# Optimization experiments

Measured on AMD Instinct MI355X. Metric: run time of the kernel, lower is better.

## Reference

```python
import jax, jax.numpy as jnp
import numpy as np

B, LC, LE, D, M = 128, 256, 1024, 256, 512
NEG = -1e9


def setup_inputs() -> dict:
    key = jax.random.key(0)
    ks = jax.random.split(key, 10)
    s = 0.02
    return {
        "criteria": jax.random.normal(ks[0], (B, LC, D), jnp.float32),
        "ehr": jax.random.normal(ks[1], (B, LE, D), jnp.float32),
        "criteria_mask": jax.random.randint(ks[2], (B, LC), 0, 2, jnp.int32),
        "ehr_mask": jax.random.randint(ks[3], (B, LE), 0, 2, jnp.int32),
        # params stored (in, out); torch Linear is x @ W.T + b
        "Wa": jax.random.normal(ks[4], (D, D), jnp.float32) * s,
        "ba": jnp.zeros((D,), jnp.float32),
        "Wr": jax.random.normal(ks[5], (2 * D, D), jnp.float32) * s,
        "br": jnp.zeros((D,), jnp.float32),
        "Wm": jax.random.normal(ks[6], (4 * D, M), jnp.float32) * s,
        "bm": jnp.zeros((M,), jnp.float32),
        "Wo": jax.random.normal(ks[7], (M, 3), jnp.float32) * s,
        "bo": jnp.zeros((3,), jnp.float32),
    }


def reference(criteria, ehr, Wa, ba, Wr, br, Wm, bm, Wo, bo,
              criteria_mask, ehr_mask):
    relu = jax.nn.relu
    c = relu(criteria @ Wa + ba)              # (B, Lc, D)
    e = relu(ehr @ Wa + ba)                   # (B, Le, D)
    align = jnp.einsum("bld,bed->ble", c, e)  # (B, Lc, Le)

    cm = criteria_mask.astype(align.dtype)
    em = ehr_mask.astype(align.dtype)
    # beta: softmax over Lc (dim=1), masked by criteria_mask along Lc
    beta = jax.nn.softmax(align + (1.0 - cm)[:, :, None] * NEG, axis=1)
    # alpha: softmax over Le (dim=1 of transposed), masked by ehr_mask along Le
    alpha = jax.nn.softmax(align + (1.0 - em)[:, None, :] * NEG, axis=2)

    # (alpha.unsqueeze(-1) * ehr.unsqueeze(1)).sum(2) == alpha @ ehr
    att_c = jnp.einsum("ble,bed->bld", alpha, ehr)        # (B, Lc, D)
    r1 = relu(jnp.concatenate([att_c, criteria], axis=-1) @ Wr + br).sum(axis=1)  # (B, D)

    # (beta.unsqueeze(-1) * criteria.unsqueeze(2)).sum(1) == beta.T @ criteria
    att_e = jnp.einsum("ble,bld->bed", beta, criteria)    # (B, Le, D)
    r2 = relu(jnp.concatenate([att_e, ehr], axis=-1) @ Wr + br).sum(axis=1)       # (B, D)

    m = jnp.concatenate([r1, r2, r1 * r2, r1 - r2], axis=-1)  # (B, 4D)
    return relu(m @ Wm + bm) @ Wo + bo                        # (B, 3)
```

## Files before the change

### kernel.cpp

```cpp
#include <hip/hip_runtime.h>
#include <hip/hip_bf16.h>

#define BB 128
#define LC 256
#define LE 1024
#define DD 256
#define MM 512

typedef short bf16x8 __attribute__((ext_vector_type(8)));
typedef unsigned short u16x8 __attribute__((ext_vector_type(8)));
typedef unsigned short u16x4 __attribute__((ext_vector_type(4)));
typedef float f32x4 __attribute__((ext_vector_type(4)));

__device__ __forceinline__ float bfu2f(unsigned short u) {
  return __uint_as_float(((unsigned int)u) << 16);
}
__device__ __forceinline__ unsigned short f2bfu(float f) {
  unsigned int x = __float_as_uint(f);
  return (unsigned short)((x + 0x7fffu + ((x >> 16) & 1u)) >> 16);
}

#define LDST 40
__device__ __forceinline__ int ldsoff(int r, int q) {
  return r * LDST + ((q ^ ((r >> 2) & 3)) << 3);
}

__device__ __forceinline__ void mma_step(const unsigned short* As, const unsigned short* Bs,
                                         f32x4 (&acc)[4][4], int wm, int wn, int lane) {
  const int lm = lane & 15, quad = lane >> 4;
  bf16x8 a[4], b[4];
#pragma unroll
  for (int i = 0; i < 4; ++i) {
    int r = wm * 64 + i * 16 + lm;
    a[i] = *(const bf16x8*)&As[ldsoff(r, quad)];
    int n = wn * 64 + i * 16 + lm;
    b[i] = *(const bf16x8*)&Bs[ldsoff(n, quad)];
  }
#pragma unroll
  for (int i = 0; i < 4; ++i)
#pragma unroll
    for (int j = 0; j < 4; ++j)
      acc[i][j] = __builtin_amdgcn_mfma_f32_16x16x32_bf16(a[i], b[j], acc[i][j], 0, 0, 0);
}

template <int MT, int NT>
__device__ __forceinline__ void mma_tiles(const unsigned short* As, const unsigned short* Bs,
                                          f32x4 (&acc)[MT][NT], int m0, int n0, int lane) {
  const int lm = lane & 15, quad = lane >> 4;
  bf16x8 a[MT], b[NT];
#pragma unroll
  for (int i = 0; i < MT; ++i)
    a[i] = *(const bf16x8*)&As[ldsoff(m0 + i * 16 + lm, quad)];
#pragma unroll
  for (int j = 0; j < NT; ++j)
    b[j] = *(const bf16x8*)&Bs[ldsoff(n0 + j * 16 + lm, quad)];
#pragma unroll
  for (int i = 0; i < MT; ++i)
#pragma unroll
    for (int j = 0; j < NT; ++j)
      acc[i][j] = __builtin_amdgcn_mfma_f32_16x16x32_bf16(a[i], b[j], acc[i][j], 0, 0, 0);
}

__device__ __forceinline__ void stage_bf16(unsigned short* S, const unsigned short* g,
                                           long ld, int tid) {
#pragma unroll
  for (int i = 0; i < 2; ++i) {
    int c = tid + i * 256;
    int r = c >> 2, q = c & 3;
    u16x8 v = *(const u16x8*)(g + (long)r * ld + q * 8);
    *(u16x8*)&S[ldsoff(r, q)] = v;
  }
}

__device__ __forceinline__ void stage_f32(unsigned short* S, const float* g, long ld, int tid) {
#pragma unroll
  for (int i = 0; i < 2; ++i) {
    int c = tid + i * 256;
    int r = c >> 2, q = c & 3;
    const float4* p = (const float4*)(g + (long)r * ld + q * 8);
    float4 v0 = p[0], v1 = p[1];
    u16x8 o;
    o[0] = f2bfu(v0.x); o[1] = f2bfu(v0.y); o[2] = f2bfu(v0.z); o[3] = f2bfu(v0.w);
    o[4] = f2bfu(v1.x); o[5] = f2bfu(v1.y); o[6] = f2bfu(v1.z); o[7] = f2bfu(v1.w);
    *(u16x8*)&S[ldsoff(r, q)] = o;
  }
}

__device__ __forceinline__ void stage512(unsigned short* S, const unsigned short* g,
                                         long ld, int tid) {
  int r = tid >> 2, q = tid & 3;
  *(u16x8*)&S[ldsoff(r, q)] = *(const u16x8*)(g + (long)r * ld + q * 8);
}

__device__ __forceinline__ void stage512x2(unsigned short* S, const unsigned short* g,
                                           long ld, int tid) {
#pragma unroll
  for (int it = 0; it < 2; ++it) {
    int c = tid + it * 512;
    int r = c >> 2, q = c & 3;
    *(u16x8*)&S[ldsoff(r, q)] = *(const u16x8*)(g + (long)r * ld + q * 8);
  }
}

__global__ void zero_kernel(float* __restrict__ p, int n) {
  int i = blockIdx.x * 256 + threadIdx.x;
  if (i < n) p[i] = 0.f;
}

__global__ void wconv_kernel(const float* __restrict__ Wa, const float* __restrict__ Wr,
                             unsigned short* __restrict__ WaT, unsigned short* __restrict__ WrT) {
  int i = blockIdx.x * 256 + threadIdx.x;
  if (i < 65536) WaT[i] = f2bfu(Wa[(i & 255) * 256 + (i >> 8)]);
  if (i < 131072) WrT[i] = f2bfu(Wr[(long)(i & 511) * 256 + (i >> 9)]);
}

__global__ void transT_kernel(const float* __restrict__ src, const int* __restrict__ mask,
                              unsigned short* __restrict__ dstT, unsigned short* __restrict__ dstN,
                              int R, int C) {
  __shared__ unsigned short T[64][72];
  const int tid = threadIdx.x, b = blockIdx.z;
  const int r0 = blockIdx.y * 64, c0 = blockIdx.x * 64;
  const float* s = src + (long)b * R * C;
  const int* mk = mask + (long)b * R;
  unsigned short* dT = dstT + (long)b * R * C;
  unsigned short* dN = dstN + (long)b * R * C;
#pragma unroll
  for (int i = 0; i < 4; ++i) {
    int r = (tid >> 4) + i * 16, c4 = tid & 15;
    float4 v = *(const float4*)(s + (long)(r0 + r) * C + c0 + c4 * 4);
    u16x4 nat;
    nat[0] = f2bfu(v.x); nat[1] = f2bfu(v.y); nat[2] = f2bfu(v.z); nat[3] = f2bfu(v.w);
    *(u16x4*)(dN + (long)(r0 + r) * C + c0 + c4 * 4) = nat;
    float g = mk[r0 + r] ? 1.f : 0.f;
    T[c4 * 4 + 0][r] = f2bfu(v.x * g);
    T[c4 * 4 + 1][r] = f2bfu(v.y * g);
    T[c4 * 4 + 2][r] = f2bfu(v.z * g);
    T[c4 * 4 + 3][r] = f2bfu(v.w * g);
  }
  __syncthreads();
#pragma unroll
  for (int j = 0; j < 2; ++j) {
    int idx = tid * 2 + j;
    int row = idx >> 3, ch = idx & 7;
    *(u16x8*)(dT + (long)(c0 + row) * R + r0 + ch * 8) = *(const u16x8*)&T[row][ch * 8];
  }
}

__global__ __launch_bounds__(256, 2) void proj_mfma(const float* __restrict__ A,
                                                    const unsigned short* __restrict__ WaT,
                                                    const float* __restrict__ ba,
                                                    unsigned short* __restrict__ out) {
  __shared__ unsigned short As[128 * LDST], Bs[128 * LDST];
  const int tid = threadIdx.x, lane = tid & 63, w = tid >> 6, wm = w >> 1, wn = w & 1;
  const long m0 = (long)blockIdx.y * 128;
  const int n0 = blockIdx.x * 128;
  f32x4 acc[4][4] = {};
  for (int k0 = 0; k0 < DD; k0 += 32) {
    stage_f32(As, A + m0 * DD + k0, DD, tid);
    stage_bf16(Bs, WaT + (long)n0 * DD + k0, DD, tid);
    __syncthreads();
    mma_step(As, Bs, acc, wm, wn, lane);
    __syncthreads();
  }
  const int lm = lane & 15, quad = lane >> 4;
#pragma unroll
  for (int i = 0; i < 4; ++i)
#pragma unroll
    for (int j = 0; j < 4; ++j) {
      int col = n0 + wn * 64 + j * 16 + lm;
      float bias = ba[col];
#pragma unroll
      for (int r = 0; r < 4; ++r) {
        long row = m0 + wm * 64 + i * 16 + quad * 4 + r;
        float v = acc[i][j][r] + bias;
        out[row * DD + col] = f2bfu(v > 0.f ? v : 0.f);
      }
    }
}

__global__ __launch_bounds__(512, 2) void attn_c_fused(
    const unsigned short* __restrict__ cB, const unsigned short* __restrict__ eB,
    const unsigned short* __restrict__ ehrTm, const int* __restrict__ em,
    unsigned short* __restrict__ attc) {
  __shared__ unsigned short AB[256 * LDST];
  __shared__ unsigned short S4[4][128 * LDST];
  __shared__ float asum_s[128];
  const int tid = threadIdx.x, lane = tid & 63, w = tid >> 6;
  const int lm = lane & 15, quad = lane >> 4;
  const int wmS = w >> 2, wnS = w & 3;
  const int wm = w >> 2, wn = w & 3;
  const int fid = blockIdx.x;
  const int lid = (fid & 7) * 32 + (fid >> 3);
  const int b = lid >> 1, m0 = (lid & 1) * 128;
  unsigned short* As = AB;
  unsigned short* Bs = AB + 128 * LDST;
  const unsigned short* Ag = cB + ((long)b * LC + m0) * DD;
  if (tid < 128) asum_s[tid] = 0.f;
  f32x4 acc[4][4] = {};
  float ap0 = 0.f, ap1 = 0.f;
  __syncthreads();
  for (int ch = 0; ch < 8; ++ch) {
    const unsigned short* Eg = eB + ((long)b * LE + ch * 128) * DD;
    f32x4 accS[4][2] = {};
    for (int k0 = 0; k0 < DD; k0 += 32) {
      stage512(As, Eg + k0, DD, tid);
      stage512(Bs, Ag + k0, DD, tid);
      __syncthreads();
      mma_tiles<4, 2>(As, Bs, accS, wmS * 64, wnS * 32, lane);
      __syncthreads();
    }
#pragma unroll
    for (int i = 0; i < 4; ++i) {
      const int Le0 = wmS * 64 + i * 16 + quad * 4;
      const int4 m4 = *(const int4*)(em + (long)b * LE + ch * 128 + Le0);
      const float em0 = m4.x ? 1.f : 0.f, em1 = m4.y ? 1.f : 0.f;
      const float em2 = m4.z ? 1.f : 0.f, em3 = m4.w ? 1.f : 0.f;
      const int kk = Le0 >> 5, wi = Le0 & 31;
      const int qq = wi >> 3, sub = wi & 7;
#pragma unroll
      for (int j = 0; j < 2; ++j) {
        const int row = wnS * 32 + j * 16 + lm;
        float e0 = __expf(accS[i][j][0]);
        float e1 = __expf(accS[i][j][1]);
        float e2 = __expf(accS[i][j][2]);
        float e3 = __expf(accS[i][j][3]);
        float s = em0 * e0 + em1 * e1 + em2 * e2 + em3 * e3;
        if (j == 0) ap0 += s; else ap1 += s;
        u16x4 pk;
        pk[0] = f2bfu(e0); pk[1] = f2bfu(e1); pk[2] = f2bfu(e2); pk[3] = f2bfu(e3);
        *(u16x4*)&S4[kk][ldsoff(row, qq) + sub] = pk;
      }
    }
    __syncthreads();
    for (int kk = 0; kk < 4; ++kk) {
      stage512x2(AB, ehrTm + (long)b * DD * LE + ch * 128 + kk * 32, LE, tid);
      __syncthreads();
      mma_tiles<4, 4>(&S4[kk][0], AB, acc, wm * 64, wn * 64, lane);
      __syncthreads();
    }
  }
  {
    float s = ap0;
    s += __shfl_xor(s, 16); s += __shfl_xor(s, 32);
    if (quad == 0) atomicAdd(&asum_s[wnS * 32 + 0 * 16 + lm], s);
    float t = ap1;
    t += __shfl_xor(t, 16); t += __shfl_xor(t, 32);
    if (quad == 0) atomicAdd(&asum_s[wnS * 32 + 1 * 16 + lm], t);
  }
  __syncthreads();
  float rs[4][4];
#pragma unroll
  for (int i = 0; i < 4; ++i)
#pragma unroll
    for (int r = 0; r < 4; ++r)
      rs[i][r] = 1.f / asum_s[wm * 64 + i * 16 + quad * 4 + r];
#pragma unroll
  for (int i = 0; i < 4; ++i)
#pragma unroll
    for (int j = 0; j < 4; ++j) {
      int col = wn * 64 + j * 16 + lm;
#pragma unroll
      for (int r = 0; r < 4; ++r) {
        int row = wm * 64 + i * 16 + quad * 4 + r;
        attc[((long)b * LC + m0 + row) * DD + col] = f2bfu(acc[i][j][r] * rs[i][r]);
      }
    }
}

__global__ __launch_bounds__(512, 2) void attn_e_fused(
    const unsigned short* __restrict__ cB, const unsigned short* __restrict__ eB,
    const unsigned short* __restrict__ critTm, const int* __restrict__ cm,
    unsigned short* __restrict__ atte) {
  __shared__ unsigned short AB[256 * LDST];
  __shared__ unsigned short S4[4][128 * LDST];
  __shared__ float bsum_s[128];
  const int tid = threadIdx.x, lane = tid & 63, w = tid >> 6;
  const int lm = lane & 15, quad = lane >> 4;
  const int wmS = w >> 2, wnS = w & 3;
  const int wm = w >> 2, wn = w & 3;
  const int fid = blockIdx.x;
  const int lid = (fid & 7) * 128 + (fid >> 3);
  const int b = lid >> 3, n0 = (lid & 7) * 128;
  unsigned short* As = AB;
  unsigned short* Bs = AB + 128 * LDST;
  const unsigned short* Eg = eB + ((long)b * LE + n0) * DD;
  if (tid < 128) bsum_s[tid] = 0.f;
  f32x4 acc[4][4] = {};
  float bp0 = 0.f, bp1 = 0.f;
  __syncthreads();
  for (int ch = 0; ch < 2; ++ch) {
    const unsigned short* Cg = cB + ((long)b * LC + ch * 128) * DD;
    f32x4 accS[4][2] = {};
    for (int k0 = 0; k0 < DD; k0 += 32) {
      stage512(As, Cg + k0, DD, tid);
      stage512(Bs, Eg + k0, DD, tid);
      __syncthreads();
      mma_tiles<4, 2>(As, Bs, accS, wmS * 64, wnS * 32, lane);
      __syncthreads();
    }
#pragma unroll
    for (int i = 0; i < 4; ++i) {
      const int Lc0 = wmS * 64 + i * 16 + quad * 4;
      const int4 m4 = *(const int4*)(cm + (long)b * LC + ch * 128 + Lc0);
      const float cm0 = m4.x ? 1.f : 0.f, cm1 = m4.y ? 1.f : 0.f;
      const float cm2 = m4.z ? 1.f : 0.f, cm3 = m4.w ? 1.f : 0.f;
      const int kk = Lc0 >> 5, wi = Lc0 & 31;
      const int qq = wi >> 3, sub = wi & 7;
#pragma unroll
      for (int j = 0; j < 2; ++j) {
        const int row = wnS * 32 + j * 16 + lm;
        float e0 = __expf(accS[i][j][0]);
        float e1 = __expf(accS[i][j][1]);
        float e2 = __expf(accS[i][j][2]);
        float e3 = __expf(accS[i][j][3]);
        float s = cm0 * e0 + cm1 * e1 + cm2 * e2 + cm3 * e3;
        if (j == 0) bp0 += s; else bp1 += s;
        u16x4 pk;
        pk[0] = f2bfu(e0); pk[1] = f2bfu(e1); pk[2] = f2bfu(e2); pk[3] = f2bfu(e3);
        *(u16x4*)&S4[kk][ldsoff(row, qq) + sub] = pk;
      }
    }
    __syncthreads();
    for (int kk = 0; kk < 4; ++kk) {
      stage512x2(AB, critTm + (long)b * DD * LC + ch * 128 + kk * 32, LC, tid);
      __syncthreads();
      mma_tiles<4, 4>(&S4[kk][0], AB, acc, wm * 64, wn * 64, lane);
      __syncthreads();
    }
  }
  {
    float s = bp0;
    s += __shfl_xor(s, 16); s += __shfl_xor(s, 32);
    if (quad == 0) atomicAdd(&bsum_s[wnS * 32 + 0 * 16 + lm], s);
    float t = bp1;
    t += __shfl_xor(t, 16); t += __shfl_xor(t, 32);
    if (quad == 0) atomicAdd(&bsum_s[wnS * 32 + 1 * 16 + lm], t);
  }
  __syncthreads();
  float rs[4][4];
#pragma unroll
  for (int i = 0; i < 4; ++i)
#pragma unroll
    for (int r = 0; r < 4; ++r)
      rs[i][r] = 1.f / bsum_s[wm * 64 + i * 16 + quad * 4 + r];
#pragma unroll
  for (int i = 0; i < 4; ++i)
#pragma unroll
    for (int j = 0; j < 4; ++j) {
      int col = wn * 64 + j * 16 + lm;
#pragma unroll
      for (int r = 0; r < 4; ++r) {
        int row = wm * 64 + i * 16 + quad * 4 + r;
        atte[((long)b * LE + n0 + row) * DD + col] = f2bfu(acc[i][j][r] * rs[i][r]);
      }
    }
}

__global__ __launch_bounds__(256, 2) void rsum_mfma(const unsigned short* __restrict__ att,
                                                    const unsigned short* __restrict__ origB,
                                                    const unsigned short* __restrict__ WrT,
                                                    const float* __restrict__ br,
                                                    float* __restrict__ rout, int Lseq) {
  __shared__ unsigned short As[128 * LDST], Bs[128 * LDST];
  __shared__ float red[2][128];
  const int tid = threadIdx.x, lane = tid & 63, w = tid >> 6, wm = w >> 1, wn = w & 1;
  const long m0 = (long)blockIdx.y * 128;
  const int n0 = blockIdx.x * 128;
  const int b = (int)(m0 / Lseq);
  f32x4 acc[4][4] = {};
  for (int k0 = 0; k0 < 2 * DD; k0 += 32) {
    if (k0 < DD)
      stage_bf16(As, att + m0 * DD + k0, DD, tid);
    else
      stage_bf16(As, origB + m0 * DD + (k0 - DD), DD, tid);
    stage_bf16(Bs, WrT + (long)n0 * (2 * DD) + k0, 2 * DD, tid);
    __syncthreads();
    mma_step(As, Bs, acc, wm, wn, lane);
    __syncthreads();
  }
  const int lm = lane & 15, quad = lane >> 4;
#pragma unroll
  for (int j = 0; j < 4; ++j) {
    int col = n0 + wn * 64 + j * 16 + lm;
    float bias = br[col];
    float s = 0.f;
#pragma unroll
    for (int i = 0; i < 4; ++i)
#pragma unroll
      for (int r = 0; r < 4; ++r) {
        float v = acc[i][j][r] + bias;
        s += v > 0.f ? v : 0.f;
      }
    s += __shfl_xor(s, 16);
    s += __shfl_xor(s, 32);
    if (quad == 0) red[wm][wn * 64 + j * 16 + lm] = s;
  }
  __syncthreads();
  if (tid < 128)
    atomicAdd(&rout[b * DD + n0 + tid], red[0][tid] + red[1][tid]);
}

__global__ void mbuild_kernel(const float* __restrict__ r1, const float* __restrict__ r2,
                              unsigned short* __restrict__ mB) {
  int i = blockIdx.x * 256 + threadIdx.x;
  int b = i >> 8, d = i & 255;
  float v1 = r1[i], v2 = r2[i];
  unsigned short* row = mB + (long)b * 1024;
  row[d] = f2bfu(v1);
  row[256 + d] = f2bfu(v2);
  row[512 + d] = f2bfu(v1 * v2);
  row[768 + d] = f2bfu(v1 - v2);
}

__global__ __launch_bounds__(256, 2) void mlp_mfma(const unsigned short* __restrict__ mB,
                                                   const float* __restrict__ Wm,
                                                   const float* __restrict__ bm,
                                                   float* __restrict__ h) {
  __shared__ unsigned short As[128 * LDST], Bs[128 * LDST];
  const int tid = threadIdx.x, lane = tid & 63, w = tid >> 6, wm = w >> 1, wn = w & 1;
  const int n0 = blockIdx.x * 128;
  f32x4 acc[4][4] = {};
  for (int k0 = 0; k0 < 4 * DD; k0 += 32) {
    stage_bf16(As, mB + k0, 4 * DD, tid);
    {
      const int dcc = tid & 7, er = tid >> 3;
#pragma unroll
      for (int i = 0; i < 4; ++i) {
        int nch = dcc + i * 8;
        float4 v = *(const float4*)(Wm + (long)(k0 + er) * MM + n0 + nch * 4);
        float vv[4] = {v.x, v.y, v.z, v.w};
#pragma unroll
        for (int q = 0; q < 4; ++q)
          Bs[ldsoff(nch * 4 + q, er >> 3) + (er & 7)] = f2bfu(vv[q]);
      }
    }
    __syncthreads();
    mma_step(As, Bs, acc, wm, wn, lane);
    __syncthreads();
  }
  const int lm = lane & 15, quad = lane >> 4;
#pragma unroll
  for (int i = 0; i < 4; ++i)
#pragma unroll
    for (int j = 0; j < 4; ++j) {
      int col = n0 + wn * 64 + j * 16 + lm;
      float bias = bm[col];
#pragma unroll
      for (int r = 0; r < 4; ++r) {
        int row = wm * 64 + i * 16 + quad * 4 + r;
        float v = acc[i][j][r] + bias;
        h[(long)row * MM + col] = v > 0.f ? v : 0.f;
      }
    }
}

__global__ void out3_kernel(const float* __restrict__ h, const float* __restrict__ Wo,
                            const float* __restrict__ bo, float* __restrict__ out) {
  const int b = blockIdx.x, tid = threadIdx.x;
  __shared__ float red[256];
  float a[3] = {0.f, 0.f, 0.f};
  for (int k = tid; k < MM; k += 256) {
    float hv = h[(long)b * MM + k];
    a[0] += hv * Wo[k * 3 + 0];
    a[1] += hv * Wo[k * 3 + 1];
    a[2] += hv * Wo[k * 3 + 2];
  }
#pragma unroll
  for (int o = 0; o < 3; ++o) {
    red[tid] = a[o]; __syncthreads();
    for (int st = 128; st > 0; st >>= 1) {
      if (tid < st) red[tid] += red[tid + st];
      __syncthreads();
    }
    if (tid == 0) out[b * 3 + o] = red[0] + bo[o];
    __syncthreads();
  }
}

extern "C" void kernel_launch(void* const* d_in, const int* in_sizes, int n_in,
                              void* d_out, int out_size, void* d_ws, size_t ws_size,
                              hipStream_t stream) {
  const float* criteria = (const float*)d_in[0];
  const float* ehr      = (const float*)d_in[1];
  const int*   cmask    = (const int*)d_in[2];
  const int*   emask    = (const int*)d_in[3];
  const float* Wa       = (const float*)d_in[4];
  const float* ba       = (const float*)d_in[5];
  const float* Wr       = (const float*)d_in[6];
  const float* br       = (const float*)d_in[7];
  const float* Wm       = (const float*)d_in[8];
  const float* bm       = (const float*)d_in[9];
  const float* Wo       = (const float*)d_in[10];
  const float* bo       = (const float*)d_in[11];
  float* out = (float*)d_out;

  char* ws = (char*)d_ws;
  unsigned short* cB     = (unsigned short*)(ws);
  unsigned short* eB     = (unsigned short*)(ws + 16777216);
  unsigned short* ehrTm  = (unsigned short*)(ws + 83886080);
  unsigned short* critTm = (unsigned short*)(ws + 150994944);
  unsigned short* ehrN   = (unsigned short*)(ws + 167772160);
  unsigned short* critN  = (unsigned short*)(ws + 234881024);
  unsigned short* attc   = (unsigned short*)(ws + 251658240);
  unsigned short* atteP  = (unsigned short*)(ws + 268435456);
  float* r1   = (float*)(ws + 335544320);
  float* r2   = (float*)(ws + 335675392);
  unsigned short* WaT = (unsigned short*)(ws + 335806464);
  unsigned short* WrT = (unsigned short*)(ws + 335937536);
  unsigned short* mB  = (unsigned short*)(ws + 336199680);
  float* hbuf         = (float*)(ws + 336461824);

  dim3 blk(256);
  zero_kernel<<<dim3(256), blk, 0, stream>>>(r1, 65536);
  wconv_kernel<<<dim3(512), blk, 0, stream>>>(Wa, Wr, WaT, WrT);
  transT_kernel<<<dim3(DD / 64, LE / 64, BB), blk, 0, stream>>>(ehr, emask, ehrTm, ehrN, LE, DD);
  transT_kernel<<<dim3(DD / 64, LC / 64, BB), blk, 0, stream>>>(criteria, cmask, critTm, critN, LC, DD);
  proj_mfma<<<dim3(2, (BB * LC) / 128), blk, 0, stream>>>(criteria, WaT, ba, cB);
  proj_mfma<<<dim3(2, (BB * LE) / 128), blk, 0, stream>>>(ehr, WaT, ba, eB);
  attn_c_fused<<<dim3(BB * (LC / 128)), dim3(512), 0, stream>>>(cB, eB, ehrTm, emask, attc);
  attn_e_fused<<<dim3(BB * (LE / 128)), dim3(512), 0, stream>>>(cB, eB, critTm, cmask, atteP);
  rsum_mfma<<<dim3(2, (BB * LC) / 128), blk, 0, stream>>>(attc, critN, WrT, br, r1, LC);
  rsum_mfma<<<dim3(2, (BB * LE) / 128), blk, 0, stream>>>(atteP, ehrN, WrT, br, r2, LE);
  mbuild_kernel<<<dim3(BB), blk, 0, stream>>>(r1, r2, mB);
  mlp_mfma<<<dim3(MM / 128), blk, 0, stream>>>(mB, Wm, bm, hbuf);
  out3_kernel<<<dim3(BB), blk, 0, stream>>>(hbuf, Wo, bo, out);
}
```

Before: 623.9 us.

## Merge attention kernels into one launch with double-buffered LDS staging

The two attention kernels become a single launch that dispatches on block index to a shared body. Global-to-LDS staging is now double-buffered, so the next k-slice, the next PV tile, or the next chunk's first slice is loaded while MFMAs run on the current buffer. This removes one barrier per step and the idle time between the two launches. It also repacks the probability tile with a new XOR swizzle, drops the old swizzle from the common LDS offset (which risks bank conflicts), and raises wave priority around MFMA bursts.

```diff
diff --git a/kernel.cpp b/kernel.cpp
--- a/kernel.cpp
+++ b/kernel.cpp
@@ -22,7 +22,7 @@
 
 #define LDST 40
 __device__ __forceinline__ int ldsoff(int r, int q) {
-  return r * LDST + ((q ^ ((r >> 2) & 3)) << 3);
+  return r * LDST + (q << 3);
 }
 
 __device__ __forceinline__ void mma_step(const unsigned short* As, const unsigned short* Bs,
@@ -54,11 +54,33 @@
 #pragma unroll
   for (int j = 0; j < NT; ++j)
     b[j] = *(const bf16x8*)&Bs[ldsoff(n0 + j * 16 + lm, quad)];
+  __builtin_amdgcn_s_setprio(1);
 #pragma unroll
   for (int i = 0; i < MT; ++i)
 #pragma unroll
     for (int j = 0; j < NT; ++j)
       acc[i][j] = __builtin_amdgcn_mfma_f32_16x16x32_bf16(a[i], b[j], acc[i][j], 0, 0, 0);
+  __builtin_amdgcn_s_setprio(0);
+}
+
+__device__ __forceinline__ void mma_pv(const unsigned short* S4c, const unsigned short* Bs,
+                                       f32x4 (&acc)[4][4], int m0, int n0, int lane) {
+  const int lm = lane & 15, quad = lane >> 4;
+  bf16x8 a[4], b[4];
+#pragma unroll
+  for (int i = 0; i < 4; ++i) {
+    int r = m0 + i * 16 + lm;
+    a[i] = *(const bf16x8*)&S4c[r * 32 + ((quad ^ ((r >> 1) & 3)) << 3)];
+    int n = n0 + i * 16 + lm;
+    b[i] = *(const bf16x8*)&Bs[ldsoff(n, quad)];
+  }
+  __builtin_amdgcn_s_setprio(1);
+#pragma unroll
+  for (int i = 0; i < 4; ++i)
+#pragma unroll
+    for (int j = 0; j < 4; ++j)
+      acc[i][j] = __builtin_amdgcn_mfma_f32_16x16x32_bf16(a[i], b[j], acc[i][j], 0, 0, 0);
+  __builtin_amdgcn_s_setprio(0);
 }
 
 __device__ __forceinline__ void stage_bf16(unsigned short* S, const unsigned short* g,
@@ -178,44 +200,44 @@
     }
 }
 
-__global__ __launch_bounds__(512, 2) void attn_c_fused(
-    const unsigned short* __restrict__ cB, const unsigned short* __restrict__ eB,
-    const unsigned short* __restrict__ ehrTm, const int* __restrict__ em,
-    unsigned short* __restrict__ attc) {
-  __shared__ unsigned short AB[256 * LDST];
-  __shared__ unsigned short S4[4][128 * LDST];
-  __shared__ float asum_s[128];
-  const int tid = threadIdx.x, lane = tid & 63, w = tid >> 6;
+__device__ void attn_body(unsigned short* L,
+                          const unsigned short* resB, const unsigned short* aSrc,
+                          const unsigned short* pvB, long pvLd, int nch,
+                          const int* mask, unsigned short* outp, int tid) {
+  const int lane = tid & 63, w = tid >> 6;
   const int lm = lane & 15, quad = lane >> 4;
   const int wmS = w >> 2, wnS = w & 3;
   const int wm = w >> 2, wn = w & 3;
-  const int fid = blockIdx.x;
-  const int lid = (fid & 7) * 32 + (fid >> 3);
-  const int b = lid >> 1, m0 = (lid & 1) * 128;
-  unsigned short* As = AB;
-  unsigned short* Bs = AB + 128 * LDST;
-  const unsigned short* Ag = cB + ((long)b * LC + m0) * DD;
-  if (tid < 128) asum_s[tid] = 0.f;
+  unsigned short* S4 = L + 20480;
+  float* asum_s = (float*)L;
   f32x4 acc[4][4] = {};
   float ap0 = 0.f, ap1 = 0.f;
+  stage512(L, aSrc, DD, tid);
+  stage512(L + 5120, resB, DD, tid);
   __syncthreads();
-  for (int ch = 0; ch < 8; ++ch) {
-    const unsigned short* Eg = eB + ((long)b * LE + ch * 128) * DD;
+  for (int ch = 0; ch < nch; ++ch) {
+    const unsigned short* Ag = aSrc + (long)ch * 128 * DD;
     f32x4 accS[4][2] = {};
-    for (int k0 = 0; k0 < DD; k0 += 32) {
-      stage512(As, Eg + k0, DD, tid);
-      stage512(Bs, Ag + k0, DD, tid);
+#pragma unroll
+    for (int s = 0; s < 8; ++s) {
+      if (s < 7) {
+        unsigned short* d = L + ((s + 1) & 1) * 10240;
+        stage512(d, Ag + (s + 1) * 32, DD, tid);
+        stage512(d + 5120, resB + (s + 1) * 32, DD, tid);
+      } else {
+        stage512x2(L, pvB + (long)ch * 128, pvLd, tid);
+      }
+      const unsigned short* base = L + (s & 1) * 10240;
+      mma_tiles<4, 2>(base, base + 5120, accS, wmS * 64, wnS * 32, lane);
       __syncthreads();
-      mma_tiles<4, 2>(As, Bs, accS, wmS * 64, wnS * 32, lane);
-      __syncthreads();
     }
 #pragma unroll
     for (int i = 0; i < 4; ++i) {
-      const int Le0 = wmS * 64 + i * 16 + quad * 4;
-      const int4 m4 = *(const int4*)(em + (long)b * LE + ch * 128 + Le0);
-      const float em0 = m4.x ? 1.f : 0.f, em1 = m4.y ? 1.f : 0.f;
-      const float em2 = m4.z ? 1.f : 0.f, em3 = m4.w ? 1.f : 0.f;
-      const int kk = Le0 >> 5, wi = Le0 & 31;
+      const int A0 = wmS * 64 + i * 16 + quad * 4;
+      const int4 m4 = *(const int4*)(mask + ch * 128 + A0);
+      const float g0 = m4.x ? 1.f : 0.f, g1 = m4.y ? 1.f : 0.f;
+      const float g2 = m4.z ? 1.f : 0.f, g3 = m4.w ? 1.f : 0.f;
+      const int kk = A0 >> 5, wi = A0 & 31;
       const int qq = wi >> 3, sub = wi & 7;
 #pragma unroll
       for (int j = 0; j < 2; ++j) {
@@ -224,28 +246,35 @@
         float e1 = __expf(accS[i][j][1]);
         float e2 = __expf(accS[i][j][2]);
         float e3 = __expf(accS[i][j][3]);
-        float s = em0 * e0 + em1 * e1 + em2 * e2 + em3 * e3;
-        if (j == 0) ap0 += s; else ap1 += s;
+        float sm = g0 * e0 + g1 * e1 + g2 * e2 + g3 * e3;
+        if (j == 0) ap0 += sm; else ap1 += sm;
         u16x4 pk;
         pk[0] = f2bfu(e0); pk[1] = f2bfu(e1); pk[2] = f2bfu(e2); pk[3] = f2bfu(e3);
-        *(u16x4*)&S4[kk][ldsoff(row, qq) + sub] = pk;
-      }
-    }
-    __syncthreads();
+        *(u16x4*)&S4[kk * 4096 + row * 32 + ((qq ^ ((row >> 1) & 3)) << 3) + sub] = pk;
+      }
+    }
+    __syncthreads();
+#pragma unroll
     for (int kk = 0; kk < 4; ++kk) {
-      stage512x2(AB, ehrTm + (long)b * DD * LE + ch * 128 + kk * 32, LE, tid);
+      if (kk < 3) {
+        stage512x2(L + ((kk + 1) & 1) * 10240, pvB + (long)ch * 128 + (kk + 1) * 32, pvLd, tid);
+      } else if (ch + 1 < nch) {
+        stage512(L, aSrc + (long)(ch + 1) * 128 * DD, DD, tid);
+        stage512(L + 5120, resB, DD, tid);
+      }
+      mma_pv(S4 + kk * 4096, L + (kk & 1) * 10240, acc, wm * 64, wn * 64, lane);
       __syncthreads();
-      mma_tiles<4, 4>(&S4[kk][0], AB, acc, wm * 64, wn * 64, lane);
-      __syncthreads();
-    }
-  }
+    }
+  }
+  if (tid < 128) asum_s[tid] = 0.f;
+  __syncthreads();
   {
     float s = ap0;
     s += __shfl_xor(s, 16); s += __shfl_xor(s, 32);
-    if (quad == 0) atomicAdd(&asum_s[wnS * 32 + 0 * 16 + lm], s);
+    if (quad == 0) atomicAdd(&asum_s[wnS * 32 + lm], s);
     float t = ap1;
     t += __shfl_xor(t, 16); t += __shfl_xor(t, 32);
-    if (quad == 0) atomicAdd(&asum_s[wnS * 32 + 1 * 16 + lm], t);
+    if (quad == 0) atomicAdd(&asum_s[wnS * 32 + 16 + lm], t);
   }
   __syncthreads();
   float rs[4][4];
@@ -262,98 +291,32 @@
 #pragma unroll
       for (int r = 0; r < 4; ++r) {
         int row = wm * 64 + i * 16 + quad * 4 + r;
-        attc[((long)b * LC + m0 + row) * DD + col] = f2bfu(acc[i][j][r] * rs[i][r]);
-      }
-    }
-}
-
-__global__ __launch_bounds__(512, 2) void attn_e_fused(
+        outp[(long)row * DD + col] = f2bfu(acc[i][j][r] * rs[i][r]);
+      }
+    }
+}
+
+__global__ __launch_bounds__(512, 2) void attn_fused(
     const unsigned short* __restrict__ cB, const unsigned short* __restrict__ eB,
-    const unsigned short* __restrict__ critTm, const int* __restrict__ cm,
-    unsigned short* __restrict__ atte) {
-  __shared__ unsigned short AB[256 * LDST];
-  __shared__ unsigned short S4[4][128 * LDST];
-  __shared__ float bsum_s[128];
-  const int tid = threadIdx.x, lane = tid & 63, w = tid >> 6;
-  const int lm = lane & 15, quad = lane >> 4;
-  const int wmS = w >> 2, wnS = w & 3;
-  const int wm = w >> 2, wn = w & 3;
-  const int fid = blockIdx.x;
-  const int lid = (fid & 7) * 128 + (fid >> 3);
-  const int b = lid >> 3, n0 = (lid & 7) * 128;
-  unsigned short* As = AB;
-  unsigned short* Bs = AB + 128 * LDST;
-  const unsigned short* Eg = eB + ((long)b * LE + n0) * DD;
-  if (tid < 128) bsum_s[tid] = 0.f;
-  f32x4 acc[4][4] = {};
-  float bp0 = 0.f, bp1 = 0.f;
-  __syncthreads();
-  for (int ch = 0; ch < 2; ++ch) {
-    const unsigned short* Cg = cB + ((long)b * LC + ch * 128) * DD;
-    f32x4 accS[4][2] = {};
-    for (int k0 = 0; k0 < DD; k0 += 32) {
-      stage512(As, Cg + k0, DD, tid);
-      stage512(Bs, Eg + k0, DD, tid);
-      __syncthreads();
-      mma_tiles<4, 2>(As, Bs, accS, wmS * 64, wnS * 32, lane);
-      __syncthreads();
-    }
-#pragma unroll
-    for (int i = 0; i < 4; ++i) {
-      const int Lc0 = wmS * 64 + i * 16 + quad * 4;
-      const int4 m4 = *(const int4*)(cm + (long)b * LC + ch * 128 + Lc0);
-      const float cm0 = m4.x ? 1.f : 0.f, cm1 = m4.y ? 1.f : 0.f;
-      const float cm2 = m4.z ? 1.f : 0.f, cm3 = m4.w ? 1.f : 0.f;
-      const int kk = Lc0 >> 5, wi = Lc0 & 31;
-      const int qq = wi >> 3, sub = wi & 7;
-#pragma unroll
-      for (int j = 0; j < 2; ++j) {
-        const int row = wnS * 32 + j * 16 + lm;
-        float e0 = __expf(accS[i][j][0]);
-        float e1 = __expf(accS[i][j][1]);
-        float e2 = __expf(accS[i][j][2]);
-        float e3 = __expf(accS[i][j][3]);
-        float s = cm0 * e0 + cm1 * e1 + cm2 * e2 + cm3 * e3;
-        if (j == 0) bp0 += s; else bp1 += s;
-        u16x4 pk;
-        pk[0] = f2bfu(e0); pk[1] = f2bfu(e1); pk[2] = f2bfu(e2); pk[3] = f2bfu(e3);
-        *(u16x4*)&S4[kk][ldsoff(row, qq) + sub] = pk;
-      }
-    }
-    __syncthreads();
-    for (int kk = 0; kk < 4; ++kk) {
-      stage512x2(AB, critTm + (long)b * DD * LC + ch * 128 + kk * 32, LC, tid);
-      __syncthreads();
-      mma_tiles<4, 4>(&S4[kk][0], AB, acc, wm * 64, wn * 64, lane);
-      __syncthreads();
-    }
-  }
-  {
-    float s = bp0;
-    s += __shfl_xor(s, 16); s += __shfl_xor(s, 32);
-    if (quad == 0) atomicAdd(&bsum_s[wnS * 32 + 0 * 16 + lm], s);
-    float t = bp1;
-    t += __shfl_xor(t, 16); t += __shfl_xor(t, 32);
-    if (quad == 0) atomicAdd(&bsum_s[wnS * 32 + 1 * 16 + lm], t);
-  }
-  __syncthreads();
-  float rs[4][4];
-#pragma unroll
-  for (int i = 0; i < 4; ++i)
-#pragma unroll
-    for (int r = 0; r < 4; ++r)
-      rs[i][r] = 1.f / bsum_s[wm * 64 + i * 16 + quad * 4 + r];
-#pragma unroll
-  for (int i = 0; i < 4; ++i)
-#pragma unroll
-    for (int j = 0; j < 4; ++j) {
-      int col = wn * 64 + j * 16 + lm;
-#pragma unroll
-      for (int r = 0; r < 4; ++r) {
-        int row = wm * 64 + i * 16 + quad * 4 + r;
-        atte[((long)b * LE + n0 + row) * DD + col] = f2bfu(acc[i][j][r] * rs[i][r]);
-      }
-    }
+    const unsigned short* __restrict__ ehrTm, const unsigned short* __restrict__ critTm,
+    const int* __restrict__ em, const int* __restrict__ cm,
+    unsigned short* __restrict__ attc, unsigned short* __restrict__ atte) {
+  __shared__ unsigned short L[36864];
+  const int tid = threadIdx.x, fid = blockIdx.x;
+  if (fid < 256) {
+    const int lid = (fid & 7) * 32 + (fid >> 3);
+    const int b = lid >> 1, m0 = (lid & 1) * 128;
+    attn_body(L, cB + ((long)b * LC + m0) * DD, eB + (long)b * LE * DD,
+              ehrTm + (long)b * DD * LE, LE, 8, em + (long)b * LE,
+              attc + ((long)b * LC + m0) * DD, tid);
+  } else {
+    const int f = fid - 256;
+    const int lid = (f & 7) * 128 + (f >> 3);
+    const int b = lid >> 3, n0 = (lid & 7) * 128;
+    attn_body(L, eB + ((long)b * LE + n0) * DD, cB + (long)b * LC * DD,
+              critTm + (long)b * DD * LC, LC, 2, cm + (long)b * LC,
+              atte + ((long)b * LE + n0) * DD, tid);
+  }
 }
 
 __global__ __launch_bounds__(256, 2) void rsum_mfma(const unsigned short* __restrict__ att,
@@ -517,8 +480,8 @@
   transT_kernel<<<dim3(DD / 64, LC / 64, BB), blk, 0, stream>>>(criteria, cmask, critTm, critN, LC, DD);
   proj_mfma<<<dim3(2, (BB * LC) / 128), blk, 0, stream>>>(criteria, WaT, ba, cB);
   proj_mfma<<<dim3(2, (BB * LE) / 128), blk, 0, stream>>>(ehr, WaT, ba, eB);
-  attn_c_fused<<<dim3(BB * (LC / 128)), dim3(512), 0, stream>>>(cB, eB, ehrTm, emask, attc);
-  attn_e_fused<<<dim3(BB * (LE / 128)), dim3(512), 0, stream>>>(cB, eB, critTm, cmask, atteP);
+  attn_fused<<<dim3(1280), dim3(512), 0, stream>>>(cB, eB, ehrTm, critTm, emask, cmask,
+                                                   attc, atteP);
   rsum_mfma<<<dim3(2, (BB * LC) / 128), blk, 0, stream>>>(attc, critN, WrT, br, r1, LC);
   rsum_mfma<<<dim3(2, (BB * LE) / 128), blk, 0, stream>>>(atteP, ehrN, WrT, br, r2, LE);
   mbuild_kernel<<<dim3(BB), blk, 0, stream>>>(r1, r2, mB);
```

Measured after the change: 694.7 us. 1.11x slower.
